# Performance work log

Measured on AMD Instinct MI355X. Metric: run time of the kernel, lower is better.

## Reference

```python
import jax, jax.numpy as jnp
import numpy as np

L = 3          # encoder layers
H, D = 12, 64  # heads, head_dim
DM = H * D     # 768
DF = 3072
WH = WW = 14
S = WH * WW + 1            # 197 tokens incl. cls
ND = (2*WH-1)*(2*WW-1) + 3  # 732 rel-pos entries
EPS = 1e-12


def _make_rel_idx():
    coords = np.stack(np.meshgrid(np.arange(WH), np.arange(WW), indexing='ij'))
    coords = coords.reshape(2, -1)                      # [2, 196]
    rel = (coords[:, :, None] - coords[:, None, :]).transpose(1, 2, 0)  # [196,196,2]
    rel[:, :, 0] += WH - 1
    rel[:, :, 1] += WW - 1
    rel[:, :, 0] *= 2 * WW - 1
    idx = np.zeros((S, S), dtype=np.int32)
    idx[1:, 1:] = rel.sum(-1)
    idx[0, :] = ND - 3
    idx[:, 0] = ND - 2
    idx[0, 0] = ND - 1
    return jnp.asarray(idx.flatten())

REL_IDX = _make_rel_idx()


def _ln(x, g, b):
    m = jnp.mean(x, -1, keepdims=True)
    v = jnp.mean(jnp.square(x - m), -1, keepdims=True)
    return (x - m) * jax.lax.rsqrt(v + EPS) * g + b


def setup_inputs() -> dict:
    key = jax.random.key(0)
    ks = iter(jax.random.split(key, 32))
    p = lambda *s: jax.random.normal(next(ks), s, jnp.float32) * 0.02
    inp = {
        'x': jax.random.normal(next(ks), (64, WH, WW, DM), jnp.float32),
        'cls': p(1, 1, DM),
        'g1': jnp.ones((L, DM)), 'b1': jnp.zeros((L, DM)),
        'Wq': p(L, DM, DM), 'bq': jnp.zeros((L, DM)),
        'Wk': p(L, DM, DM),
        'Wv': p(L, DM, DM), 'bv': jnp.zeros((L, DM)),
        'rel_tbl': p(L, ND, H),
        'Wo': p(L, DM, DM), 'bo': jnp.zeros((L, DM)),
        'lam1': jnp.full((L, DM), 0.1),
        'g2': jnp.ones((L, DM)), 'b2': jnp.zeros((L, DM)),
        'Wi': p(L, DM, DF), 'bi': jnp.zeros((L, DF)),
        'Wmo': p(L, DF, DM), 'bmo': jnp.zeros((L, DM)),
        'lam2': jnp.full((L, DM), 0.1),
    }
    return inp


def reference(x, cls, g1, b1, Wq, bq, Wk, Wv, bv, rel_tbl, Wo, bo, lam1,
              g2, b2, Wi, bi, Wmo, bmo, lam2):
    B = x.shape[0]
    # patchemb: NHWC -> NCHW -> [B, C, HW] -> [B, HW, C], prepend cls token
    t = jnp.transpose(x, (0, 3, 1, 2)).reshape(B, DM, WH * WW)
    t = jnp.transpose(t, (0, 2, 1))
    h = jnp.concatenate([jnp.broadcast_to(cls, (B, 1, DM)), t], axis=1)  # [B,S,DM]

    scale = 1.0 / np.sqrt(D)
    for i in range(L):
        r = h
        hn = _ln(h, g1[i], b1[i])
        q = (hn @ Wq[i] + bq[i]).reshape(B, S, H, D)
        k = (hn @ Wk[i]).reshape(B, S, H, D)
        v = (hn @ Wv[i] + bv[i]).reshape(B, S, H, D)
        scores = jnp.einsum('bqhd,bkhd->bhqk', q, k) * scale   # [B,H,S,S]
        rel = rel_tbl[i][REL_IDX].reshape(S, S, H)             # gather bias table
        scores = scores + jnp.transpose(rel, (2, 0, 1))[None]
        probs = jax.nn.softmax(scores, axis=-1)
        ctx = jnp.einsum('bhqk,bkhd->bqhd', probs, v).reshape(B, S, DM)
        h = r + (ctx @ Wo[i] + bo[i]) * lam1[i]
        r = h
        hn = _ln(h, g2[i], b2[i])
        ff = jax.nn.gelu(hn @ Wi[i] + bi[i], approximate=False) @ Wmo[i] + bmo[i]
        h = r + ff * lam2[i]
    return h  # final encoder output [B, S, DM]
```

## Files before the change

kernel.cpp:

```cpp
#include <hip/hip_runtime.h>

#define DMM 768
#define DFF 3072
#define NH  12
#define HD  64
#define SQ  197
#define BA  64
#define NDD 732
#define MROWS (BA*SQ)
#define MPAD  12672
#define PCOLS 224
#define KS2   72
#define VTS   232
#define QS    2304
#define BIASN (NH*208*208)

typedef unsigned short u16;
typedef __bf16 bf16x8 __attribute__((ext_vector_type(8)));
typedef float  f32x4  __attribute__((ext_vector_type(4)));
typedef unsigned short us8 __attribute__((ext_vector_type(8)));

__device__ __forceinline__ float b2f(u16 u) {
    unsigned v = ((unsigned)u) << 16;
    float f; __builtin_memcpy(&f, &v, 4); return f;
}
__device__ __forceinline__ u16 f2b(float f) {
    unsigned v; __builtin_memcpy(&v, &f, 4);
    unsigned r = v + 0x7FFFu + ((v >> 16) & 1u);
    return (u16)(r >> 16);
}
__device__ __forceinline__ float gelu_exact(float x) {
    return 0.5f * x * (1.0f + erff(x * 0.70710678118654752f));
}
__device__ __forceinline__ void gload16(const u16* g, u16* l) {
    __builtin_amdgcn_global_load_lds(
        (const __attribute__((address_space(1))) unsigned int*)(g),
        (__attribute__((address_space(3))) unsigned int*)(l), 16, 0, 0);
}
__device__ __forceinline__ void hard_barrier() {
    asm volatile("s_waitcnt lgkmcnt(0)" ::: "memory");
    __builtin_amdgcn_s_barrier();
}

__global__ void patch_k(const float* __restrict__ x, const float* __restrict__ cls,
                        float* __restrict__ h) {
    long idx = (long)blockIdx.x * 256 + threadIdx.x;
    if (idx >= (long)MPAD * DMM) return;
    long r = idx / DMM; int c = (int)(idx % DMM);
    float v = 0.0f;
    if (r < MROWS) {
        int b = (int)(r / SQ), s = (int)(r % SQ);
        v = (s == 0) ? cls[c] : x[((long)b * 196 + (s - 1)) * DMM + c];
    }
    h[idx] = v;
}

__global__ void out_k(const float* __restrict__ h, float* __restrict__ out) {
    long idx = (long)blockIdx.x * 256 + threadIdx.x;
    if (idx < (long)MROWS * DMM) out[idx] = h[idx];
}

__global__ __launch_bounds__(256) void tcast_k(const float* __restrict__ in,
                                               u16* __restrict__ out,
                                               int Kd, int Nd) {
    __shared__ float t[32][33];
    int k0 = blockIdx.x * 32, n0 = blockIdx.y * 32;
    int tx = threadIdx.x & 31, ty = threadIdx.x >> 5;
    #pragma unroll
    for (int i = 0; i < 4; ++i)
        t[tx][ty + 8 * i] = in[(long)(k0 + ty + 8 * i) * Nd + n0 + tx];
    __syncthreads();
    #pragma unroll
    for (int i = 0; i < 4; ++i)
        out[(long)(n0 + ty + 8 * i) * Kd + k0 + tx] = f2b(t[ty + 8 * i][tx]);
}

__global__ __launch_bounds__(256) void tcast4_k(
    const float* __restrict__ s0, const float* __restrict__ s1,
    const float* __restrict__ s2, const float* __restrict__ s3,
    u16* __restrict__ d0, u16* __restrict__ d1,
    u16* __restrict__ d2, u16* __restrict__ d3) {
    __shared__ float t[32][33];
    int z = blockIdx.z;
    const float* in = (z == 0) ? s0 : (z == 1) ? s1 : (z == 2) ? s2 : s3;
    u16* out = (z == 0) ? d0 : (z == 1) ? d1 : (z == 2) ? d2 : d3;
    int k0 = blockIdx.x * 32, n0 = blockIdx.y * 32;
    int tx = threadIdx.x & 31, ty = threadIdx.x >> 5;
    #pragma unroll
    for (int i = 0; i < 4; ++i)
        t[tx][ty + 8 * i] = in[(long)(k0 + ty + 8 * i) * DMM + n0 + tx];
    __syncthreads();
    #pragma unroll
    for (int i = 0; i < 4; ++i)
        out[(long)(n0 + ty + 8 * i) * DMM + k0 + tx] = f2b(t[ty + 8 * i][tx]);
}

__global__ __launch_bounds__(256) void ln_k(const float* __restrict__ h,
                                            const float* __restrict__ g,
                                            const float* __restrict__ b,
                                            u16* __restrict__ hn) {
    int row = blockIdx.x, tid = threadIdx.x;
    const float* hr = h + (long)row * DMM;
    float x0 = hr[tid], x1 = hr[tid + 256], x2 = hr[tid + 512];
    float s = x0 + x1 + x2, sq = x0 * x0 + x1 * x1 + x2 * x2;
    #pragma unroll
    for (int m = 32; m > 0; m >>= 1) {
        s  += __shfl_xor(s,  m, 64);
        sq += __shfl_xor(sq, m, 64);
    }
    __shared__ float ls[4], lq[4];
    int w = tid >> 6;
    if ((tid & 63) == 0) { ls[w] = s; lq[w] = sq; }
    __syncthreads();
    s  = ls[0] + ls[1] + ls[2] + ls[3];
    sq = lq[0] + lq[1] + lq[2] + lq[3];
    float mean = s * (1.0f / DMM);
    float var  = fmaxf(sq * (1.0f / DMM) - mean * mean, 0.0f);
    float rs = rsqrtf(var + 1e-12f);
    u16* hnr = hn + (long)row * DMM;
    hnr[tid]       = f2b((x0 - mean) * rs * g[tid]       + b[tid]);
    hnr[tid + 256] = f2b((x1 - mean) * rs * g[tid + 256] + b[tid + 256]);
    hnr[tid + 512] = f2b((x2 - mean) * rs * g[tid + 512] + b[tid + 512]);
}

template <int EPI>
__global__ __launch_bounds__(256) void gemm_bt(
    const u16* __restrict__ A, const u16* __restrict__ BT,
    const float* __restrict__ bias, u16* __restrict__ outB,
    float* __restrict__ hio, const float* __restrict__ lam,
    int K, int N) {
    __shared__ __align__(16) u16 pool[24576];
    int tid = threadIdx.x;
    int w = tid >> 6, lane = tid & 63;
    int wr = w >> 1, wc = w & 1;
    int m16 = lane & 15;
    int kq  = (lane >> 4) * 8;
    int kq4 = (lane >> 4) * 4;

    int nwg = gridDim.x, bid = blockIdx.x;
    int qd = nwg >> 3, rm = nwg & 7;
    int xcd = bid & 7, seq = bid >> 3;
    int wg = (xcd < rm ? xcd * (qd + 1) : rm * (qd + 1) + (xcd - rm) * qd) + seq;
    int ntn = N >> 7;
    long m0 = (long)(wg / ntn) * 128;
    long n0 = (long)(wg % ntn) * 128;

    f32x4 acc[4][4] = {};

    int row_a = tid >> 2;
    int col_a = (tid & 3) * 8;
    const u16* gA0 = &A[(m0 + row_a) * (long)K + col_a];
    const u16* gA1 = &A[(m0 + 64 + row_a) * (long)K + col_a];
    const u16* gB0 = &BT[(n0 + row_a) * (long)K + col_a];
    const u16* gB1 = &BT[(n0 + 64 + row_a) * (long)K + col_a];
    int wo = w * 512;

    u16* const b0 = pool;
    u16* const b1 = pool + 8192;
    u16* const b2 = pool + 16384;

    auto stage = [&](int k, u16* buf) {
        int k0 = k << 5;
        gload16(gA0 + k0, buf + wo);
        gload16(gA1 + k0, buf + 2048 + wo);
        gload16(gB0 + k0, buf + 4096 + wo);
        gload16(gB1 + k0, buf + 6144 + wo);
    };
    auto compute = [&](const u16* buf) {
        bf16x8 af[4], bf[4];
        #pragma unroll
        for (int i = 0; i < 4; ++i)
            af[i] = *(const bf16x8*)&buf[(wr * 64 + i * 16 + m16) * 32 + kq];
        #pragma unroll
        for (int j = 0; j < 4; ++j)
            bf[j] = *(const bf16x8*)&buf[4096 + (wc * 64 + j * 16 + m16) * 32 + kq];
        __builtin_amdgcn_s_setprio(1);
        #pragma unroll
        for (int i = 0; i < 4; ++i)
            #pragma unroll
            for (int j = 0; j < 4; ++j)
                acc[i][j] = __builtin_amdgcn_mfma_f32_16x16x32_bf16(
                    af[i], bf[j], acc[i][j], 0, 0, 0);
        __builtin_amdgcn_s_setprio(0);
    };

    const int nsteps = K >> 5;
    stage(0, b0);
    stage(1, b1);
    const int niter = nsteps / 3 - 1;
    for (int it = 0; it < niter; ++it) {
        int k = it * 3;
        asm volatile("s_waitcnt vmcnt(4)" ::: "memory");
        __builtin_amdgcn_s_barrier();
        stage(k + 2, b2);
        compute(b0);
        asm volatile("s_waitcnt vmcnt(4)" ::: "memory");
        __builtin_amdgcn_s_barrier();
        stage(k + 3, b0);
        compute(b1);
        asm volatile("s_waitcnt vmcnt(4)" ::: "memory");
        __builtin_amdgcn_s_barrier();
        stage(k + 4, b1);
        compute(b2);
    }
    asm volatile("s_waitcnt vmcnt(4)" ::: "memory");
    __builtin_amdgcn_s_barrier();
    stage(nsteps - 1, b2);
    compute(b0);
    asm volatile("s_waitcnt vmcnt(4)" ::: "memory");
    __builtin_amdgcn_s_barrier();
    compute(b1);
    asm volatile("s_waitcnt vmcnt(0)" ::: "memory");
    __builtin_amdgcn_s_barrier();
    compute(b2);

    hard_barrier();
    float* Cs = (float*)pool;
    float bcol[4];
    #pragma unroll
    for (int j = 0; j < 4; ++j)
        bcol[j] = bias ? bias[n0 + wc * 64 + j * 16 + m16] : 0.0f;
    int et4 = tid * 4;
    int colr = et4 & 127;
    f32x4 lam4 = {};
    if (EPI == 2) lam4 = *(const f32x4*)&lam[n0 + colr];

    #pragma unroll
    for (int p = 0; p < 2; ++p) {
        if (p) hard_barrier();
        if (wr == p) {
            #pragma unroll
            for (int i = 0; i < 4; ++i)
                #pragma unroll
                for (int j = 0; j < 4; ++j)
                    #pragma unroll
                    for (int r = 0; r < 4; ++r)
                        Cs[(i * 16 + kq4 + r) * 132 + wc * 64 + j * 16 + m16] =
                            acc[i][j][r] + bcol[j];
        }
        hard_barrier();
        #pragma unroll
        for (int k = 0; k < 8; ++k) {
            int e0 = k * 1024 + et4;
            int row = e0 >> 7;
            f32x4 v = *(const f32x4*)&Cs[row * 132 + colr];
            long gi = (m0 + p * 64 + row) * (long)N + n0 + colr;
            if (EPI == 0) {
                uint2 o;
                o.x = (unsigned)f2b(v[0]) | ((unsigned)f2b(v[1]) << 16);
                o.y = (unsigned)f2b(v[2]) | ((unsigned)f2b(v[3]) << 16);
                *(uint2*)&outB[gi] = o;
            } else if (EPI == 1) {
                uint2 o;
                o.x = (unsigned)f2b(gelu_exact(v[0])) | ((unsigned)f2b(gelu_exact(v[1])) << 16);
                o.y = (unsigned)f2b(gelu_exact(v[2])) | ((unsigned)f2b(gelu_exact(v[3])) << 16);
                *(uint2*)&outB[gi] = o;
            } else {
                f32x4 hv = *(f32x4*)&hio[gi];
                #pragma unroll
                for (int t = 0; t < 4; ++t) hv[t] += v[t] * lam4[t];
                *(f32x4*)&hio[gi] = hv;
            }
        }
    }
}

__device__ __forceinline__ int relidx(int q, int k) {
    if (q == 0 && k == 0) return NDD - 1;
    if (k == 0) return NDD - 2;
    if (q == 0) return NDD - 3;
    int a = q - 1, c = k - 1;
    int dh = a / 14 - c / 14 + 13;
    int dw = a % 14 - c % 14 + 13;
    return dh * 27 + dw;
}

__global__ void bias_k(const float* __restrict__ rel, float* __restrict__ bias,
                       const float* __restrict__ bq, const float* __restrict__ bv,
                       float* __restrict__ bqkv) {
    int idx = blockIdx.x * 256 + threadIdx.x;
    if (idx < BIASN) {
        int hh = idx / (208 * 208);
        int r = (idx / 208) % 208, c = idx % 208;
        float v = 0.0f;
        if (r < SQ && c < SQ) v = rel[relidx(r, c) * NH + hh];
        bias[idx] = v;
    } else {
        int i = idx - BIASN;
        if (i < QS)
            bqkv[i] = (i < 768) ? bq[i] : ((i < 1536) ? 0.0f : bv[i - 1536]);
    }
}

__global__ __launch_bounds__(256) void attn_qk(
    const u16* __restrict__ QKV, const float* __restrict__ bias,
    u16* __restrict__ P) {
    int bh = blockIdx.x;
    int b = bh / NH, hh = bh % NH;
    __shared__ u16 Ks[208 * KS2];
    int tid = threadIdx.x, w = tid >> 6, lane = tid & 63;
    long base = ((long)b * SQ) * QS + hh * HD;
    const u16* Qp = QKV;
    const u16* Kp = QKV + 768;
    u16* Pb = P + (long)bh * 208 * PCOLS;
    for (int idx = tid; idx < 208 * 16; idx += 256)
        Pb[(idx >> 4) * PCOLS + 208 + (idx & 15)] = 0;
    for (int idx = tid; idx < 208 * 8; idx += 256) {
        int row = idx >> 3, dg = (idx & 7) * 8;
        us8 kv = {};
        if (row < SQ) kv = *(const us8*)&Kp[base + (long)row * QS + dg];
        *(us8*)&Ks[row * KS2 + dg] = kv;
    }
    __syncthreads();
    int m16 = lane & 15, quad = lane >> 4;
    int kq8 = quad * 8, q4 = quad * 4;
    const float* bh_bias = bias + (long)hh * 208 * 208;
    for (int t = w; t < 13; t += 4) {
        int m0 = t * 16;
        int qrow = m0 + m16; if (qrow > SQ - 1) qrow = SQ - 1;
        bf16x8 a0 = *(const bf16x8*)&Qp[base + (long)qrow * QS + kq8];
        bf16x8 a1 = *(const bf16x8*)&Qp[base + (long)qrow * QS + 32 + kq8];
        f32x4 sc[13];
        #pragma unroll
        for (int n = 0; n < 13; ++n) {
            bf16x8 b0 = *(const bf16x8*)&Ks[(n * 16 + m16) * KS2 + kq8];
            bf16x8 b1 = *(const bf16x8*)&Ks[(n * 16 + m16) * KS2 + 32 + kq8];
            f32x4 z = {};
            z = __builtin_amdgcn_mfma_f32_16x16x32_bf16(a0, b0, z, 0, 0, 0);
            z = __builtin_amdgcn_mfma_f32_16x16x32_bf16(a1, b1, z, 0, 0, 0);
            sc[n] = z;
        }
        float mx[4] = {-3e38f, -3e38f, -3e38f, -3e38f};
        #pragma unroll
        for (int n = 0; n < 13; ++n) {
            int col = n * 16 + m16;
            bool valid = col < SQ;
            #pragma unroll
            for (int r = 0; r < 4; ++r) {
                float v = sc[n][r] * 0.125f + bh_bias[(m0 + q4 + r) * 208 + col];
                v = valid ? v : -3e38f;
                sc[n][r] = v;
                mx[r] = fmaxf(mx[r], v);
            }
        }
        #pragma unroll
        for (int r = 0; r < 4; ++r)
            #pragma unroll
            for (int msk = 1; msk < 16; msk <<= 1)
                mx[r] = fmaxf(mx[r], __shfl_xor(mx[r], msk, 64));
        float sum[4] = {0, 0, 0, 0};
        #pragma unroll
        for (int n = 0; n < 13; ++n)
            #pragma unroll
            for (int r = 0; r < 4; ++r) {
                float e = __expf(sc[n][r] - mx[r]);
                sc[n][r] = e;
                sum[r] += e;
            }
        #pragma unroll
        for (int r = 0; r < 4; ++r)
            #pragma unroll
            for (int msk = 1; msk < 16; msk <<= 1)
                sum[r] += __shfl_xor(sum[r], msk, 64);
        float inv[4];
        #pragma unroll
        for (int r = 0; r < 4; ++r) inv[r] = 1.0f / sum[r];
        #pragma unroll
        for (int n = 0; n < 13; ++n) {
            int col = n * 16 + m16;
            #pragma unroll
            for (int r = 0; r < 4; ++r)
                Pb[(m0 + q4 + r) * PCOLS + col] = f2b(sc[n][r] * inv[r]);
        }
    }
}

__global__ __launch_bounds__(256) void attn_pv(
    const u16* __restrict__ P, const u16* __restrict__ QKV,
    u16* __restrict__ ctx) {
    int bh = blockIdx.x;
    int b = bh / NH, hh = bh % NH;
    __shared__ u16 Vt[64 * VTS];
    int tid = threadIdx.x, w = tid >> 6, lane = tid & 63;
    long base  = ((long)b * SQ) * QS + 1536 + hh * HD;
    long basec = ((long)b * SQ) * DMM + hh * HD;
    const u16* Vp = QKV;
    for (int idx = tid; idx < 224 * 8; idx += 256) {
        int row = idx >> 3, dg = (idx & 7) * 8;
        us8 vv = {};
        if (row < SQ) vv = *(const us8*)&Vp[base + (long)row * QS + dg];
        #pragma unroll
        for (int j = 0; j < 8; ++j) Vt[(dg + j) * VTS + row] = vv[j];
    }
    __syncthreads();
    const u16* Pb = P + (long)bh * 208 * PCOLS;
    int m16 = lane & 15, quad = lane >> 4;
    int kq8 = quad * 8, q4 = quad * 4;
    for (int t = w; t < 13; t += 4) {
        int m0 = t * 16;
        f32x4 co[4] = {};
        #pragma unroll
        for (int ks = 0; ks < 7; ++ks) {
            bf16x8 ap = *(const bf16x8*)&Pb[(m0 + m16) * PCOLS + ks * 32 + kq8];
            #pragma unroll
            for (int n = 0; n < 4; ++n) {
                bf16x8 bv = *(const bf16x8*)&Vt[(n * 16 + m16) * VTS + ks * 32 + kq8];
                co[n] = __builtin_amdgcn_mfma_f32_16x16x32_bf16(ap, bv, co[n], 0, 0, 0);
            }
        }
        #pragma unroll
        for (int n = 0; n < 4; ++n) {
            int col = n * 16 + m16;
            #pragma unroll
            for (int r = 0; r < 4; ++r) {
                int qr = m0 + q4 + r;
                if (qr < SQ) ctx[basec + (long)qr * DMM + col] = f2b(co[n][r]);
            }
        }
    }
}

extern "C" void kernel_launch(void* const* d_in, const int* in_sizes, int n_in,
                              void* d_out, int out_size, void* d_ws, size_t ws_size,
                              hipStream_t stream) {
    const float* x    = (const float*)d_in[0];
    const float* cls  = (const float*)d_in[1];
    const float* g1   = (const float*)d_in[2];
    const float* b1   = (const float*)d_in[3];
    const float* Wq   = (const float*)d_in[4];
    const float* bq   = (const float*)d_in[5];
    const float* Wk   = (const float*)d_in[6];
    const float* Wv   = (const float*)d_in[7];
    const float* bv   = (const float*)d_in[8];
    const float* rel  = (const float*)d_in[9];
    const float* Wo   = (const float*)d_in[10];
    const float* bo   = (const float*)d_in[11];
    const float* lam1 = (const float*)d_in[12];
    const float* g2   = (const float*)d_in[13];
    const float* b2   = (const float*)d_in[14];
    const float* Wi   = (const float*)d_in[15];
    const float* bi   = (const float*)d_in[16];
    const float* Wmo  = (const float*)d_in[17];
    const float* bmo  = (const float*)d_in[18];
    const float* lam2 = (const float*)d_in[19];

    char* p = (char*)d_ws;
    auto alloc = [&](size_t bytes) -> void* {
        void* r = (void*)p;
        p += (bytes + 255) & ~(size_t)255;
        return r;
    };
    float* h     = (float*)alloc((size_t)MPAD * DMM * 4);
    u16*   hn    = (u16*)alloc((size_t)MPAD * DMM * 2);
    u16*   qkvb  = (u16*)alloc((size_t)MPAD * QS * 2);
    u16*   ffh   = (u16*)alloc((size_t)MPAD * DFF * 2);
    u16*   WqkvT = (u16*)alloc((size_t)QS * DMM * 2);
    u16*   WoT   = (u16*)alloc((size_t)DMM * DMM * 2);
    u16*   WiT   = (u16*)alloc((size_t)DMM * DFF * 2);
    u16*   WmoT  = (u16*)alloc((size_t)DFF * DMM * 2);
    float* biasb = (float*)alloc((size_t)NH * 208 * 208 * 4);
    float* bqkv  = (float*)alloc((size_t)QS * 4);
    u16*   ctxb  = hn;
    u16*   Pbuf  = ffh;

    patch_k<<<((long)MPAD * DMM + 255) / 256, 256, 0, stream>>>(x, cls, h);

    dim3 tg4(DMM / 32, DMM / 32, 4);
    dim3 tg2(DMM / 32, DFF / 32);
    dim3 tg3(DFF / 32, DMM / 32);
    int gqkv = (MPAD / 128) * (QS / 128);
    int g6   = (MPAD / 128) * (DMM / 128);
    int g24  = (MPAD / 128) * (DFF / 128);

    for (int i = 0; i < 3; ++i) {
        size_t wofs  = (size_t)i * DMM * DMM;
        size_t wofs2 = (size_t)i * DMM * DFF;
        tcast4_k<<<tg4, 256, 0, stream>>>(Wq + wofs, Wk + wofs, Wv + wofs, Wo + wofs,
                                          WqkvT, WqkvT + 768 * DMM,
                                          WqkvT + 2 * 768 * DMM, WoT);
        tcast_k<<<tg2, 256, 0, stream>>>(Wi + wofs2, WiT, DMM, DFF);
        tcast_k<<<tg3, 256, 0, stream>>>(Wmo + wofs2, WmoT, DFF, DMM);
        bias_k<<<(BIASN + QS + 255) / 256, 256, 0, stream>>>(
            rel + (size_t)i * NDD * NH, biasb, bq + i * DMM, bv + i * DMM, bqkv);

        ln_k<<<MPAD, 256, 0, stream>>>(h, g1 + i * DMM, b1 + i * DMM, hn);
        gemm_bt<0><<<gqkv, 256, 0, stream>>>(hn, WqkvT, bqkv, qkvb, nullptr, nullptr, DMM, QS);
        attn_qk<<<BA * NH, 256, 0, stream>>>(qkvb, biasb, Pbuf);
        attn_pv<<<BA * NH, 256, 0, stream>>>(Pbuf, qkvb, ctxb);
        gemm_bt<2><<<g6, 256, 0, stream>>>(ctxb, WoT, bo + i * DMM, nullptr, h, lam1 + i * DMM, DMM, DMM);
        ln_k<<<MPAD, 256, 0, stream>>>(h, g2 + i * DMM, b2 + i * DMM, hn);
        gemm_bt<1><<<g24, 256, 0, stream>>>(hn, WiT, bi + i * DFF, ffh, nullptr, nullptr, DMM, DFF);
        gemm_bt<2><<<g6, 256, 0, stream>>>(ffh, WmoT, bmo + i * DMM, nullptr, h, lam2 + i * DMM, DFF, DMM);
    }

    out_k<<<((long)MROWS * DMM + 255) / 256, 256, 0, stream>>>(h, (float*)d_out);
}
```

Measured before the change: 1.378 ms.

## Fuse patch embed with first LayerNorm, write output from last GEMM, double-buffer GEMM

Patch embedding and the first LayerNorm are merged into one kernel, and the final residual GEMM writes straight to the output buffer, so the separate patch and copy kernels go away. The GEMM main loop also changes from a three-buffer LDS pipeline to a two-buffer one with extra barriers. The change drops the s_setprio hints and the padded 132 stride in the epilogue LDS tile. The smaller LDS footprint could allow more blocks per CU, but the shallower pipeline, extra barriers and likely bank conflicts in the epilogue may slow the dominant GEMMs.

```diff
diff --git a/kernel.cpp b/kernel.cpp
--- a/kernel.cpp
+++ b/kernel.cpp
@@ -20,10 +20,6 @@
 typedef float  f32x4  __attribute__((ext_vector_type(4)));
 typedef unsigned short us8 __attribute__((ext_vector_type(8)));
 
-__device__ __forceinline__ float b2f(u16 u) {
-    unsigned v = ((unsigned)u) << 16;
-    float f; __builtin_memcpy(&f, &v, 4); return f;
-}
 __device__ __forceinline__ u16 f2b(float f) {
     unsigned v; __builtin_memcpy(&v, &f, 4);
     unsigned r = v + 0x7FFFu + ((v >> 16) & 1u);
@@ -42,66 +38,19 @@
     __builtin_amdgcn_s_barrier();
 }
 
-__global__ void patch_k(const float* __restrict__ x, const float* __restrict__ cls,
-                        float* __restrict__ h) {
-    long idx = (long)blockIdx.x * 256 + threadIdx.x;
-    if (idx >= (long)MPAD * DMM) return;
-    long r = idx / DMM; int c = (int)(idx % DMM);
-    float v = 0.0f;
-    if (r < MROWS) {
-        int b = (int)(r / SQ), s = (int)(r % SQ);
-        v = (s == 0) ? cls[c] : x[((long)b * 196 + (s - 1)) * DMM + c];
-    }
-    h[idx] = v;
-}
-
-__global__ void out_k(const float* __restrict__ h, float* __restrict__ out) {
-    long idx = (long)blockIdx.x * 256 + threadIdx.x;
-    if (idx < (long)MROWS * DMM) out[idx] = h[idx];
-}
-
-__global__ __launch_bounds__(256) void tcast_k(const float* __restrict__ in,
-                                               u16* __restrict__ out,
-                                               int Kd, int Nd) {
-    __shared__ float t[32][33];
-    int k0 = blockIdx.x * 32, n0 = blockIdx.y * 32;
-    int tx = threadIdx.x & 31, ty = threadIdx.x >> 5;
-    #pragma unroll
-    for (int i = 0; i < 4; ++i)
-        t[tx][ty + 8 * i] = in[(long)(k0 + ty + 8 * i) * Nd + n0 + tx];
-    __syncthreads();
-    #pragma unroll
-    for (int i = 0; i < 4; ++i)
-        out[(long)(n0 + ty + 8 * i) * Kd + k0 + tx] = f2b(t[ty + 8 * i][tx]);
-}
-
-__global__ __launch_bounds__(256) void tcast4_k(
-    const float* __restrict__ s0, const float* __restrict__ s1,
-    const float* __restrict__ s2, const float* __restrict__ s3,
-    u16* __restrict__ d0, u16* __restrict__ d1,
-    u16* __restrict__ d2, u16* __restrict__ d3) {
-    __shared__ float t[32][33];
-    int z = blockIdx.z;
-    const float* in = (z == 0) ? s0 : (z == 1) ? s1 : (z == 2) ? s2 : s3;
-    u16* out = (z == 0) ? d0 : (z == 1) ? d1 : (z == 2) ? d2 : d3;
-    int k0 = blockIdx.x * 32, n0 = blockIdx.y * 32;
-    int tx = threadIdx.x & 31, ty = threadIdx.x >> 5;
-    #pragma unroll
-    for (int i = 0; i < 4; ++i)
-        t[tx][ty + 8 * i] = in[(long)(k0 + ty + 8 * i) * DMM + n0 + tx];
-    __syncthreads();
-    #pragma unroll
-    for (int i = 0; i < 4; ++i)
-        out[(long)(n0 + ty + 8 * i) * DMM + k0 + tx] = f2b(t[ty + 8 * i][tx]);
-}
-
-__global__ __launch_bounds__(256) void ln_k(const float* __restrict__ h,
-                                            const float* __restrict__ g,
-                                            const float* __restrict__ b,
-                                            u16* __restrict__ hn) {
+__global__ __launch_bounds__(256) void patchln_k(
+    const float* __restrict__ x, const float* __restrict__ cls,
+    const float* __restrict__ g, const float* __restrict__ b,
+    float* __restrict__ h, u16* __restrict__ hn) {
     int row = blockIdx.x, tid = threadIdx.x;
-    const float* hr = h + (long)row * DMM;
-    float x0 = hr[tid], x1 = hr[tid + 256], x2 = hr[tid + 512];
+    float x0 = 0.0f, x1 = 0.0f, x2 = 0.0f;
+    if (row < MROWS) {
+        int bb = row / SQ, s = row % SQ;
+        const float* src = (s == 0) ? cls : &x[((long)bb * 196 + (s - 1)) * DMM];
+        x0 = src[tid]; x1 = src[tid + 256]; x2 = src[tid + 512];
+    }
+    float* hr = h + (long)row * DMM;
+    hr[tid] = x0; hr[tid + 256] = x1; hr[tid + 512] = x2;
     float s = x0 + x1 + x2, sq = x0 * x0 + x1 * x1 + x2 * x2;
     #pragma unroll
     for (int m = 32; m > 0; m >>= 1) {
@@ -123,13 +72,76 @@
     hnr[tid + 512] = f2b((x2 - mean) * rs * g[tid + 512] + b[tid + 512]);
 }
 
+__global__ __launch_bounds__(256) void tcast_k(const float* __restrict__ in,
+                                               u16* __restrict__ out,
+                                               int Kd, int Nd) {
+    __shared__ float t[32][33];
+    int k0 = blockIdx.x * 32, n0 = blockIdx.y * 32;
+    int tx = threadIdx.x & 31, ty = threadIdx.x >> 5;
+    #pragma unroll
+    for (int i = 0; i < 4; ++i)
+        t[tx][ty + 8 * i] = in[(long)(k0 + ty + 8 * i) * Nd + n0 + tx];
+    __syncthreads();
+    #pragma unroll
+    for (int i = 0; i < 4; ++i)
+        out[(long)(n0 + ty + 8 * i) * Kd + k0 + tx] = f2b(t[ty + 8 * i][tx]);
+}
+
+__global__ __launch_bounds__(256) void tcast4_k(
+    const float* __restrict__ s0, const float* __restrict__ s1,
+    const float* __restrict__ s2, const float* __restrict__ s3,
+    u16* __restrict__ d0, u16* __restrict__ d1,
+    u16* __restrict__ d2, u16* __restrict__ d3) {
+    __shared__ float t[32][33];
+    int z = blockIdx.z;
+    const float* in = (z == 0) ? s0 : (z == 1) ? s1 : (z == 2) ? s2 : s3;
+    u16* out = (z == 0) ? d0 : (z == 1) ? d1 : (z == 2) ? d2 : d3;
+    int k0 = blockIdx.x * 32, n0 = blockIdx.y * 32;
+    int tx = threadIdx.x & 31, ty = threadIdx.x >> 5;
+    #pragma unroll
+    for (int i = 0; i < 4; ++i)
+        t[tx][ty + 8 * i] = in[(long)(k0 + ty + 8 * i) * DMM + n0 + tx];
+    __syncthreads();
+    #pragma unroll
+    for (int i = 0; i < 4; ++i)
+        out[(long)(n0 + ty + 8 * i) * DMM + k0 + tx] = f2b(t[ty + 8 * i][tx]);
+}
+
+__global__ __launch_bounds__(256) void ln_k(const float* __restrict__ h,
+                                            const float* __restrict__ g,
+                                            const float* __restrict__ b,
+                                            u16* __restrict__ hn) {
+    int row = blockIdx.x, tid = threadIdx.x;
+    const float* hr = h + (long)row * DMM;
+    float x0 = hr[tid], x1 = hr[tid + 256], x2 = hr[tid + 512];
+    float s = x0 + x1 + x2, sq = x0 * x0 + x1 * x1 + x2 * x2;
+    #pragma unroll
+    for (int m = 32; m > 0; m >>= 1) {
+        s  += __shfl_xor(s,  m, 64);
+        sq += __shfl_xor(sq, m, 64);
+    }
+    __shared__ float ls[4], lq[4];
+    int w = tid >> 6;
+    if ((tid & 63) == 0) { ls[w] = s; lq[w] = sq; }
+    __syncthreads();
+    s  = ls[0] + ls[1] + ls[2] + ls[3];
+    sq = lq[0] + lq[1] + lq[2] + lq[3];
+    float mean = s * (1.0f / DMM);
+    float var  = fmaxf(sq * (1.0f / DMM) - mean * mean, 0.0f);
+    float rs = rsqrtf(var + 1e-12f);
+    u16* hnr = hn + (long)row * DMM;
+    hnr[tid]       = f2b((x0 - mean) * rs * g[tid]       + b[tid]);
+    hnr[tid + 256] = f2b((x1 - mean) * rs * g[tid + 256] + b[tid + 256]);
+    hnr[tid + 512] = f2b((x2 - mean) * rs * g[tid + 512] + b[tid + 512]);
+}
+
 template <int EPI>
 __global__ __launch_bounds__(256) void gemm_bt(
     const u16* __restrict__ A, const u16* __restrict__ BT,
     const float* __restrict__ bias, u16* __restrict__ outB,
     float* __restrict__ hio, const float* __restrict__ lam,
-    int K, int N) {
-    __shared__ __align__(16) u16 pool[24576];
+    float* __restrict__ hout, int K, int N) {
+    __shared__ __align__(16) u16 pool[16384];
     int tid = threadIdx.x;
     int w = tid >> 6, lane = tid & 63;
     int wr = w >> 1, wc = w & 1;
@@ -157,7 +169,6 @@
 
     u16* const b0 = pool;
     u16* const b1 = pool + 8192;
-    u16* const b2 = pool + 16384;
 
     auto stage = [&](int k, u16* buf) {
         int k0 = k << 5;
@@ -174,45 +185,36 @@
         #pragma unroll
         for (int j = 0; j < 4; ++j)
             bf[j] = *(const bf16x8*)&buf[4096 + (wc * 64 + j * 16 + m16) * 32 + kq];
-        __builtin_amdgcn_s_setprio(1);
         #pragma unroll
         for (int i = 0; i < 4; ++i)
             #pragma unroll
             for (int j = 0; j < 4; ++j)
                 acc[i][j] = __builtin_amdgcn_mfma_f32_16x16x32_bf16(
                     af[i], bf[j], acc[i][j], 0, 0, 0);
-        __builtin_amdgcn_s_setprio(0);
     };
 
     const int nsteps = K >> 5;
     stage(0, b0);
-    stage(1, b1);
-    const int niter = nsteps / 3 - 1;
-    for (int it = 0; it < niter; ++it) {
-        int k = it * 3;
+    for (int ks = 0; ks < nsteps - 2; ks += 2) {
+        stage(ks + 1, b1);
         asm volatile("s_waitcnt vmcnt(4)" ::: "memory");
         __builtin_amdgcn_s_barrier();
-        stage(k + 2, b2);
         compute(b0);
+        hard_barrier();
+        stage(ks + 2, b0);
         asm volatile("s_waitcnt vmcnt(4)" ::: "memory");
         __builtin_amdgcn_s_barrier();
-        stage(k + 3, b0);
         compute(b1);
-        asm volatile("s_waitcnt vmcnt(4)" ::: "memory");
-        __builtin_amdgcn_s_barrier();
-        stage(k + 4, b1);
-        compute(b2);
-    }
+        hard_barrier();
+    }
+    stage(nsteps - 1, b1);
     asm volatile("s_waitcnt vmcnt(4)" ::: "memory");
     __builtin_amdgcn_s_barrier();
-    stage(nsteps - 1, b2);
     compute(b0);
-    asm volatile("s_waitcnt vmcnt(4)" ::: "memory");
+    hard_barrier();
+    asm volatile("s_waitcnt vmcnt(0)" ::: "memory");
     __builtin_amdgcn_s_barrier();
     compute(b1);
-    asm volatile("s_waitcnt vmcnt(0)" ::: "memory");
-    __builtin_amdgcn_s_barrier();
-    compute(b2);
 
     hard_barrier();
     float* Cs = (float*)pool;
@@ -235,7 +237,7 @@
                 for (int j = 0; j < 4; ++j)
                     #pragma unroll
                     for (int r = 0; r < 4; ++r)
-                        Cs[(i * 16 + kq4 + r) * 132 + wc * 64 + j * 16 + m16] =
+                        Cs[(i * 16 + kq4 + r) * 128 + wc * 64 + j * 16 + m16] =
                             acc[i][j][r] + bcol[j];
         }
         hard_barrier();
@@ -243,8 +245,9 @@
         for (int k = 0; k < 8; ++k) {
             int e0 = k * 1024 + et4;
             int row = e0 >> 7;
-            f32x4 v = *(const f32x4*)&Cs[row * 132 + colr];
-            long gi = (m0 + p * 64 + row) * (long)N + n0 + colr;
+            f32x4 v = *(const f32x4*)&Cs[row * 128 + colr];
+            long grow = m0 + p * 64 + row;
+            long gi = grow * (long)N + n0 + colr;
             if (EPI == 0) {
                 uint2 o;
                 o.x = (unsigned)f2b(v[0]) | ((unsigned)f2b(v[1]) << 16);
@@ -260,6 +263,8 @@
                 #pragma unroll
                 for (int t = 0; t < 4; ++t) hv[t] += v[t] * lam4[t];
                 *(f32x4*)&hio[gi] = hv;
+                if (hout != nullptr && grow < MROWS)
+                    *(f32x4*)&hout[gi] = hv;
             }
         }
     }
@@ -463,14 +468,14 @@
     u16*   ctxb  = hn;
     u16*   Pbuf  = ffh;
 
-    patch_k<<<((long)MPAD * DMM + 255) / 256, 256, 0, stream>>>(x, cls, h);
-
     dim3 tg4(DMM / 32, DMM / 32, 4);
     dim3 tg2(DMM / 32, DFF / 32);
     dim3 tg3(DFF / 32, DMM / 32);
     int gqkv = (MPAD / 128) * (QS / 128);
     int g6   = (MPAD / 128) * (DMM / 128);
     int g24  = (MPAD / 128) * (DFF / 128);
+
+    patchln_k<<<MPAD, 256, 0, stream>>>(x, cls, g1, b1, h, hn);
 
     for (int i = 0; i < 3; ++i) {
         size_t wofs  = (size_t)i * DMM * DMM;
@@ -483,15 +488,15 @@
         bias_k<<<(BIASN + QS + 255) / 256, 256, 0, stream>>>(
             rel + (size_t)i * NDD * NH, biasb, bq + i * DMM, bv + i * DMM, bqkv);
 
-        ln_k<<<MPAD, 256, 0, stream>>>(h, g1 + i * DMM, b1 + i * DMM, hn);
-        gemm_bt<0><<<gqkv, 256, 0, stream>>>(hn, WqkvT, bqkv, qkvb, nullptr, nullptr, DMM, QS);
+        if (i > 0)
+            ln_k<<<MPAD, 256, 0, stream>>>(h, g1 + i * DMM, b1 + i * DMM, hn);
+        gemm_bt<0><<<gqkv, 256, 0, stream>>>(hn, WqkvT, bqkv, qkvb, nullptr, nullptr, nullptr, DMM, QS);
         attn_qk<<<BA * NH, 256, 0, stream>>>(qkvb, biasb, Pbuf);
         attn_pv<<<BA * NH, 256, 0, stream>>>(Pbuf, qkvb, ctxb);
-        gemm_bt<2><<<g6, 256, 0, stream>>>(ctxb, WoT, bo + i * DMM, nullptr, h, lam1 + i * DMM, DMM, DMM);
+        gemm_bt<2><<<g6, 256, 0, stream>>>(ctxb, WoT, bo + i * DMM, nullptr, h, lam1 + i * DMM, nullptr, DMM, DMM);
         ln_k<<<MPAD, 256, 0, stream>>>(h, g2 + i * DMM, b2 + i * DMM, hn);
-        gemm_bt<1><<<g24, 256, 0, stream>>>(hn, WiT, bi + i * DFF, ffh, nullptr, nullptr, DMM, DFF);
-        gemm_bt<2><<<g6, 256, 0, stream>>>(ffh, WmoT, bmo + i * DMM, nullptr, h, lam2 + i * DMM, DFF, DMM);
-    }
-
-    out_k<<<((long)MROWS * DMM + 255) / 256, 256, 0, stream>>>(h, (float*)d_out);
-}
+        gemm_bt<1><<<g24, 256, 0, stream>>>(hn, WiT, bi + i * DFF, ffh, nullptr, nullptr, nullptr, DMM, DFF);
+        gemm_bt<2><<<g6, 256, 0, stream>>>(ffh, WmoT, bmo + i * DMM, nullptr, h, lam2 + i * DMM,
+                                           (i == 2) ? (float*)d_out : nullptr, DFF, DMM);
+    }
+}
```

After: 1.330 ms. 1.04x faster.
